# Kernel optimization log

Hardware: AMD Instinct MI355X
Metric: run time of the kernel (lower is better)

The kernel has to match this reference:

```python
import jax, jax.numpy as jnp
import numpy as np

N_NODES = 50000
N_EDGES = 800000
H, D_IN, D_OUT = 4, 256, 64


def setup_inputs() -> dict:
    key = jax.random.key(0)
    ks = jax.random.split(key, 7)
    x = jax.random.normal(ks[0], (N_NODES, D_IN), dtype=jnp.float32)
    idx = jax.random.randint(ks[1], (2, N_EDGES), 0, N_NODES, dtype=jnp.int32)
    elem = jax.random.uniform(ks[2], (N_EDGES,), dtype=jnp.float32)
    Ws = jax.random.normal(ks[3], (H, D_IN, D_OUT), dtype=jnp.float32) * 0.05
    bs = jax.random.normal(ks[4], (H, D_OUT), dtype=jnp.float32) * 0.05
    aw = jax.random.normal(ks[5], (H, 2 * D_OUT + 1), dtype=jnp.float32) * 0.05
    ab = jax.random.normal(ks[6], (H,), dtype=jnp.float32) * 0.05
    return {"x": x, "idx": idx, "elem": elem, "Ws": Ws, "bs": bs, "aw": aw, "ab": ab}


def reference(x, idx, elem, Ws, bs, aw, ab):
    N = x.shape[0]
    O = Ws.shape[-1]
    # per-head MLP (num_mlp_layers=1 -> single Linear): [H, N, O]
    feats = jnp.einsum('nd,hdo->hno', x, Ws) + bs[:, None, :]
    # attention linear on concat(src, dst, elem): split weights instead of
    # materializing the [E, 2O+1] concat; math is identical.
    aw_src, aw_dst, aw_e = aw[:, :O], aw[:, O:2 * O], aw[:, 2 * O]
    a_s = jnp.einsum('hno,ho->hn', feats, aw_src)   # [H, N]
    a_d = jnp.einsum('hno,ho->hn', feats, aw_dst)   # [H, N]
    src, dst = idx[0], idx[1]
    score = a_s[:, src] + a_d[:, dst] + aw_e[:, None] * elem[None, :] + ab[:, None]
    w = jnp.exp(-jax.nn.relu(score / 20.0))        # [H, E], in (0, 1]
    dst_f = feats[:, dst]                          # [H, E, O] gather
    seg = lambda vals: jax.ops.segment_sum(vals, src, num_segments=N)
    pooled = jax.vmap(lambda wi, fi: seg(wi[:, None] * fi))(w, dst_f)  # [H, N, O]
    row_sum = jax.vmap(lambda wi: seg(wi))(w)                          # [H, N]
    out = pooled / row_sum[:, :, None]
    # concat heads along feature dim: [N, H*O]
    return jnp.transpose(out, (1, 0, 2)).reshape(N, H * O)
```

## Files before the change

kernel.cpp:

```cpp
#include <hip/hip_runtime.h>
#include <math.h>

constexpr int DIN = 256;
constexpr int H   = 4;
constexpr int O   = 64;
constexpr int HO  = H * O;
constexpr int AWS = 2 * O + 1;
constexpr int CAP = 3072;
constexpr int HEB = 4096;

typedef __bf16 bf16x8 __attribute__((ext_vector_type(8)));
typedef __bf16 bf16x4 __attribute__((ext_vector_type(4)));
typedef float  f32x4  __attribute__((ext_vector_type(4)));

__device__ __forceinline__ float bf2f(unsigned short u) {
    union { unsigned int i; float f; } c;
    c.i = ((unsigned int)u) << 16;
    return c.f;
}

__global__ __launch_bounds__(256) void k_prep(const float* __restrict__ Ws,
    __bf16* __restrict__ Bt)
{
    const int i = blockIdx.x * 256 + threadIdx.x;
    const int k = i & 255;
    const int n = i >> 8;
    Bt[n * 256 + k] = (__bf16)Ws[(n >> 6) * (DIN * O) + k * O + (n & 63)];
}

__global__ __launch_bounds__(256) void k_gemm_hist(const float* __restrict__ x,
    const __bf16* __restrict__ Bt, const float* __restrict__ bs,
    const float* __restrict__ aw, int N, int GB,
    __bf16* __restrict__ F, float* __restrict__ a_sT, float* __restrict__ a_dT,
    const int* __restrict__ idx, int E, int* __restrict__ rank,
    int* __restrict__ hist, int NB, int NBIN)
{
    __shared__ union SM {
        __bf16 As[64][DIN + 8];
        int    lhist[64 * (DIN + 8) / 2];
    } sm;
    const int b = blockIdx.x;
    const int t = threadIdx.x;

    if (b >= GB) {
        for (int k = t; k < NBIN; k += 256) sm.lhist[k] = 0;
        __syncthreads();
        const int base_e = (b - GB) * HEB + t;
        #pragma unroll
        for (int i = 0; i < HEB / 256; ++i) {
            const int e = base_e + i * 256;
            if (e < E) {
                const int s = idx[e];
                rank[e] = atomicAdd(&sm.lhist[s >> 6], 1);
            }
        }
        __syncthreads();
        const int bh = b - GB;
        for (int k = t; k < NBIN; k += 256)
            hist[(size_t)k * NB + bh] = sm.lhist[k];
        return;
    }

    const int w    = t >> 6;
    const int lane = t & 63;
    const int c15  = lane & 15;
    const int quad = lane >> 4;
    const int n0   = b * 64;

    #pragma unroll
    for (int i = 0; i < 16; ++i) {
        const int r   = i * 4 + w;
        const int row = n0 + r;
        float4 xv = make_float4(0.f, 0.f, 0.f, 0.f);
        if (row < N) xv = *(const float4*)&x[(size_t)row * DIN + lane * 4];
        bf16x4 pv = { (__bf16)xv.x, (__bf16)xv.y, (__bf16)xv.z, (__bf16)xv.w };
        *(bf16x4*)&sm.As[r][lane * 4] = pv;
    }
    __syncthreads();

    f32x4 acc[4][4] = {};
    const __bf16* BtW = Bt + (size_t)(w * 64) * 256;
    const int kq = quad * 8;

    #pragma unroll
    for (int k0 = 0; k0 < DIN; k0 += 32) {
        bf16x8 afr[4], bfr[4];
        #pragma unroll
        for (int rt = 0; rt < 4; ++rt)
            afr[rt] = *(const bf16x8*)&sm.As[rt * 16 + c15][k0 + kq];
        #pragma unroll
        for (int ct = 0; ct < 4; ++ct)
            bfr[ct] = *(const bf16x8*)&BtW[(size_t)(ct * 16 + c15) * 256 + k0 + kq];
        #pragma unroll
        for (int rt = 0; rt < 4; ++rt)
            #pragma unroll
            for (int ct = 0; ct < 4; ++ct)
                acc[rt][ct] = __builtin_amdgcn_mfma_f32_16x16x32_bf16(
                    afr[rt], bfr[ct], acc[rt][ct], 0, 0, 0);
    }

    const int h = w;
    float bsv[4], awsv[4], awdv[4];
    #pragma unroll
    for (int ct = 0; ct < 4; ++ct) {
        const int col = ct * 16 + c15;
        bsv[ct]  = bs[w * 64 + col];
        awsv[ct] = aw[h * AWS + col];
        awdv[ct] = aw[h * AWS + O + col];
    }

    #pragma unroll
    for (int rt = 0; rt < 4; ++rt) {
        float psum[4] = {0.f, 0.f, 0.f, 0.f};
        float pdum[4] = {0.f, 0.f, 0.f, 0.f};
        #pragma unroll
        for (int ct = 0; ct < 4; ++ct) {
            #pragma unroll
            for (int reg = 0; reg < 4; ++reg) {
                const float f = acc[rt][ct][reg] + bsv[ct];
                const int row = n0 + rt * 16 + quad * 4 + reg;
                if (row < N)
                    F[(size_t)row * HO + w * 64 + ct * 16 + c15] = (__bf16)f;
                psum[reg] = fmaf(f, awsv[ct], psum[reg]);
                pdum[reg] = fmaf(f, awdv[ct], pdum[reg]);
            }
        }
        #pragma unroll
        for (int reg = 0; reg < 4; ++reg) {
            float v = psum[reg], u = pdum[reg];
            #pragma unroll
            for (int off = 1; off < 16; off <<= 1) {
                v += __shfl_xor(v, off, 64);
                u += __shfl_xor(u, off, 64);
            }
            const int row = n0 + rt * 16 + quad * 4 + reg;
            if (c15 == 0 && row < N) {
                a_sT[row * H + h] = v;
                a_dT[row * H + h] = u;
            }
        }
    }
}

__global__ __launch_bounds__(256) void k_scan1(int* __restrict__ data,
    int* __restrict__ bsum, int T)
{
    __shared__ int wsum[4], woff[4];
    const int t = threadIdx.x, b = blockIdx.x;
    const int lane = t & 63, w = t >> 6;
    const int i0 = b * 1024 + t * 4;

    int4 v = make_int4(0, 0, 0, 0);
    if (i0 + 3 < T) v = *(const int4*)&data[i0];
    else {
        if (i0     < T) v.x = data[i0];
        if (i0 + 1 < T) v.y = data[i0 + 1];
        if (i0 + 2 < T) v.z = data[i0 + 2];
    }
    const int tot = v.x + v.y + v.z + v.w;
    int s = tot;
    #pragma unroll
    for (int off = 1; off < 64; off <<= 1) {
        const int u = __shfl_up(s, off, 64);
        if (lane >= off) s += u;
    }
    if (lane == 63) wsum[w] = s;
    __syncthreads();
    if (t == 0) {
        int run = 0;
        #pragma unroll
        for (int j = 0; j < 4; ++j) { woff[j] = run; run += wsum[j]; }
        bsum[b] = run;
    }
    __syncthreads();
    const int e0 = s - tot + woff[w];
    int4 o;
    o.x = e0; o.y = e0 + v.x; o.z = o.y + v.y; o.w = o.z + v.z;
    if (i0 + 3 < T) *(int4*)&data[i0] = o;
    else {
        if (i0     < T) data[i0]     = o.x;
        if (i0 + 1 < T) data[i0 + 1] = o.y;
        if (i0 + 2 < T) data[i0 + 2] = o.z;
    }
}

__global__ __launch_bounds__(256) void k_scan2(int* __restrict__ data, int n)
{
    __shared__ int wsum[4], woff[4];
    const int t = threadIdx.x;
    const int lane = t & 63, w = t >> 6;
    const int i0 = t * 4;

    int4 v = make_int4(0, 0, 0, 0);
    if (i0 + 3 < n) v = *(const int4*)&data[i0];
    else {
        if (i0     < n) v.x = data[i0];
        if (i0 + 1 < n) v.y = data[i0 + 1];
        if (i0 + 2 < n) v.z = data[i0 + 2];
    }
    const int tot = v.x + v.y + v.z + v.w;
    int s = tot;
    #pragma unroll
    for (int off = 1; off < 64; off <<= 1) {
        const int u = __shfl_up(s, off, 64);
        if (lane >= off) s += u;
    }
    if (lane == 63) wsum[w] = s;
    __syncthreads();
    if (t == 0) {
        int run = 0;
        #pragma unroll
        for (int j = 0; j < 4; ++j) { woff[j] = run; run += wsum[j]; }
    }
    __syncthreads();
    const int e0 = s - tot + woff[w];
    int4 o;
    o.x = e0; o.y = e0 + v.x; o.z = o.y + v.y; o.w = o.z + v.z;
    if (i0 + 3 < n) *(int4*)&data[i0] = o;
    else {
        if (i0     < n) data[i0]     = o.x;
        if (i0 + 1 < n) data[i0 + 1] = o.y;
        if (i0 + 2 < n) data[i0 + 2] = o.z;
    }
}

__global__ __launch_bounds__(256) void k_scatter(const int* __restrict__ idx,
    const float* __restrict__ elem, const int* __restrict__ rank,
    const int* __restrict__ hist, const int* __restrict__ hsum,
    int NB, int E, int2* __restrict__ csr)
{
    const int e = blockIdx.x * 256 + threadIdx.x;
    if (e >= E) return;
    const int s = idx[e];
    const int d = idx[E + e];
    const int i = (s >> 6) * NB + (e / HEB);
    const int pos = hist[i] + hsum[i >> 10] + rank[e];
    csr[pos] = make_int2((int)(((unsigned)s << 16) | (unsigned)d),
                         __float_as_int(elem[e]));
}

__global__ __launch_bounds__(256) void k_binsort(const int* __restrict__ hist,
    const int* __restrict__ hsum, int NB, int NBIN, int N, int E,
    int* __restrict__ row_ptr, int2* __restrict__ csr)
{
    __shared__ int2 recs[CAP];
    __shared__ int h[64];
    __shared__ int cur[64];
    const int k = blockIdx.x;
    const int t = threadIdx.x;

    const int i0 = k * NB;
    const int S = hist[i0] + hsum[i0 >> 10];
    int Snext = E;
    if (k + 1 < NBIN) {
        const int i1 = (k + 1) * NB;
        Snext = hist[i1] + hsum[i1 >> 10];
    }
    int cnt = Snext - S;
    if (cnt > CAP) cnt = CAP;

    if (t < 64) h[t] = 0;
    __syncthreads();
    for (int j = t; j < cnt; j += 256) {
        const int2 r = csr[S + j];
        recs[j] = r;
        atomicAdd(&h[((unsigned)r.x >> 16) & 63], 1);
    }
    __syncthreads();
    if (t < 64) {
        const int v = h[t];
        int s = v;
        #pragma unroll
        for (int off = 1; off < 64; off <<= 1) {
            const int u = __shfl_up(s, off, 64);
            if (t >= off) s += u;
        }
        const int excl = s - v;
        const int node = k * 64 + t;
        if (node < N)     row_ptr[node] = S + excl;
        if (node == N - 1) row_ptr[N]   = S + excl + v;
        cur[t] = S + excl;
    }
    __syncthreads();
    for (int j = t; j < cnt; j += 256) {
        const int2 r = recs[j];
        const int pos = atomicAdd(&cur[((unsigned)r.x >> 16) & 63], 1);
        csr[pos] = make_int2((int)((unsigned)r.x & 0xFFFFu), r.y);
    }
}

__global__ __launch_bounds__(256) void k_gather(const int* __restrict__ row_ptr,
    const int2* __restrict__ csr, const float* __restrict__ a_sT,
    const float* __restrict__ a_dT, const float* __restrict__ aw,
    const float* __restrict__ ab, const __bf16* __restrict__ F,
    float* __restrict__ out, int N)
{
    __shared__ int2  s_rec[4][64];
    __shared__ float s_w[4][256];

    const int t    = threadIdx.x;
    const int wv   = t >> 6;
    const int lane = t & 63;
    const int n    = blockIdx.x * 4 + wv;
    if (n >= N) return;
    const int h16  = lane >> 4;

    const int beg = row_ptr[n];
    const int end = row_ptr[n + 1];

    const float4 as4 = *(const float4*)&a_sT[n * 4];
    const float4 ab4 = *(const float4*)&ab[0];
    const float4 awe4 = make_float4(aw[0 * AWS + 2 * O], aw[1 * AWS + 2 * O],
                                    aw[2 * AWS + 2 * O], aw[3 * AWS + 2 * O]);

    float4 acc = make_float4(0.f, 0.f, 0.f, 0.f);
    float  rs  = 0.f;
    const __bf16* __restrict__ Fl = F + lane * 4;

    for (int base = beg; base < end; base += 64) {
        const int cnt = min(64, end - base);
        if (lane < cnt) {
            const int2 r = csr[base + lane];
            s_rec[wv][lane] = r;
            const float el = __int_as_float(r.y);
            const float4 ad = *(const float4*)&a_dT[r.x * 4];
            float4 w4;
            w4.x = __expf(-fmaxf((as4.x + ad.x + awe4.x * el + ab4.x) * 0.05f, 0.f));
            w4.y = __expf(-fmaxf((as4.y + ad.y + awe4.y * el + ab4.y) * 0.05f, 0.f));
            w4.z = __expf(-fmaxf((as4.z + ad.z + awe4.z * el + ab4.z) * 0.05f, 0.f));
            w4.w = __expf(-fmaxf((as4.w + ad.w + awe4.w * el + ab4.w) * 0.05f, 0.f));
            *(float4*)&s_w[wv][lane * 4] = w4;
        }
        __threadfence_block();

        int j = 0;
        for (; j + 4 <= cnt; j += 4) {
            const int d0 = s_rec[wv][j + 0].x;
            const int d1 = s_rec[wv][j + 1].x;
            const int d2 = s_rec[wv][j + 2].x;
            const int d3 = s_rec[wv][j + 3].x;
            const float w0 = s_w[wv][(j + 0) * 4 + h16];
            const float w1 = s_w[wv][(j + 1) * 4 + h16];
            const float w2 = s_w[wv][(j + 2) * 4 + h16];
            const float w3 = s_w[wv][(j + 3) * 4 + h16];
            const ushort4 f0 = *(const ushort4*)&Fl[(size_t)d0 * HO];
            const ushort4 f1 = *(const ushort4*)&Fl[(size_t)d1 * HO];
            const ushort4 f2 = *(const ushort4*)&Fl[(size_t)d2 * HO];
            const ushort4 f3 = *(const ushort4*)&Fl[(size_t)d3 * HO];
            acc.x = fmaf(w0, bf2f(f0.x), acc.x);
            acc.y = fmaf(w0, bf2f(f0.y), acc.y);
            acc.z = fmaf(w0, bf2f(f0.z), acc.z);
            acc.w = fmaf(w0, bf2f(f0.w), acc.w);
            acc.x = fmaf(w1, bf2f(f1.x), acc.x);
            acc.y = fmaf(w1, bf2f(f1.y), acc.y);
            acc.z = fmaf(w1, bf2f(f1.z), acc.z);
            acc.w = fmaf(w1, bf2f(f1.w), acc.w);
            acc.x = fmaf(w2, bf2f(f2.x), acc.x);
            acc.y = fmaf(w2, bf2f(f2.y), acc.y);
            acc.z = fmaf(w2, bf2f(f2.z), acc.z);
            acc.w = fmaf(w2, bf2f(f2.w), acc.w);
            acc.x = fmaf(w3, bf2f(f3.x), acc.x);
            acc.y = fmaf(w3, bf2f(f3.y), acc.y);
            acc.z = fmaf(w3, bf2f(f3.z), acc.z);
            acc.w = fmaf(w3, bf2f(f3.w), acc.w);
            rs += w0 + w1 + w2 + w3;
        }
        for (; j < cnt; ++j) {
            const int d = s_rec[wv][j].x;
            const float w = s_w[wv][j * 4 + h16];
            const ushort4 fv = *(const ushort4*)&Fl[(size_t)d * HO];
            acc.x = fmaf(w, bf2f(fv.x), acc.x);
            acc.y = fmaf(w, bf2f(fv.y), acc.y);
            acc.z = fmaf(w, bf2f(fv.z), acc.z);
            acc.w = fmaf(w, bf2f(fv.w), acc.w);
            rs += w;
        }
    }

    const float inv = 1.f / rs;
    float4 o = make_float4(acc.x * inv, acc.y * inv, acc.z * inv, acc.w * inv);
    *(float4*)&out[(size_t)n * HO + lane * 4] = o;
}

extern "C" void kernel_launch(void* const* d_in, const int* in_sizes, int n_in,
                              void* d_out, int out_size, void* d_ws, size_t ws_size,
                              hipStream_t stream)
{
    const float* x    = (const float*)d_in[0];
    const int*   idx  = (const int*)d_in[1];
    const float* elem = (const float*)d_in[2];
    const float* Ws   = (const float*)d_in[3];
    const float* bs   = (const float*)d_in[4];
    const float* aw   = (const float*)d_in[5];
    const float* ab   = (const float*)d_in[6];

    const int N    = in_sizes[0] / DIN;
    const int E    = in_sizes[1] / 2;
    const int GB   = (N + 63) / 64;
    const int NB   = (E + HEB - 1) / HEB;
    const int NBIN = (N + 63) / 64;
    const int T    = NBIN * NB;
    const int nb1  = (T + 1023) / 1024;

    __bf16* F      = (__bf16*)d_ws;
    float* a_sT    = (float*)(F + (size_t)N * HO);
    float* a_dT    = a_sT + (size_t)N * H;
    int*   hist    = (int*)(a_dT + (size_t)N * H);
    int*   hsum    = hist + T;
    int*   row_ptr = hsum + (nb1 + 1);
    int*   rank    = row_ptr + (N + 1);
    size_t off = (size_t)((char*)(rank + E) - (char*)d_ws);
    off = (off + 15) & ~(size_t)15;
    int2*  csr     = (int2*)((char*)d_ws + off);
    __bf16* Bt     = (__bf16*)(csr + E);
    float* out     = (float*)d_out;

    k_prep<<<256, 256, 0, stream>>>(Ws, Bt);
    k_gemm_hist<<<GB + NB, 256, 0, stream>>>(x, Bt, bs, aw, N, GB,
                                             F, a_sT, a_dT, idx, E,
                                             rank, hist, NB, NBIN);
    k_scan1<<<nb1, 256, 0, stream>>>(hist, hsum, T);
    k_scan2<<<1, 256, 0, stream>>>(hsum, nb1);
    k_scatter<<<(E + 255) / 256, 256, 0, stream>>>(idx, elem, rank, hist,
                                                   hsum, NB, E, csr);
    k_binsort<<<NBIN, 256, 0, stream>>>(hist, hsum, NB, NBIN, N, E,
                                        row_ptr, csr);
    k_gather<<<(N + 3) / 4, 256, 0, stream>>>(row_ptr, csr, a_sT, a_dT,
                                              aw, ab, F, out, N);
}
```

Baseline: 240.3 us.

## Compute edge weights in binsort and widen gather unroll to eight edges

Edge attention weights are now computed in the binsort kernel, which already touches every edge, and written with the destination index into separate CSR arrays. The gather kernel then only loads precomputed weights instead of gathering a_dT and evaluating exp per edge. The gather inner loop is also unrolled to eight independent feature loads for more memory-level parallelism. The cost is extra global traffic: a 16-byte weight record plus a 4-byte index per edge written and read back, instead of the 8-byte record, along with more workspace and higher register pressure in gather.

```diff
diff --git a/kernel.cpp b/kernel.cpp
--- a/kernel.cpp
+++ b/kernel.cpp
@@ -241,9 +241,13 @@
 
 __global__ __launch_bounds__(256) void k_binsort(const int* __restrict__ hist,
     const int* __restrict__ hsum, int NB, int NBIN, int N, int E,
-    int* __restrict__ row_ptr, int2* __restrict__ csr)
+    const float* __restrict__ a_sT, const float* __restrict__ a_dT,
+    const float* __restrict__ aw, const float* __restrict__ ab,
+    int* __restrict__ row_ptr, const int2* __restrict__ csr,
+    int* __restrict__ csrd, float4* __restrict__ csrw)
 {
     __shared__ int2 recs[CAP];
+    __shared__ float4 s_as[64];
     __shared__ int h[64];
     __shared__ int cur[64];
     const int k = blockIdx.x;
@@ -259,7 +263,12 @@
     int cnt = Snext - S;
     if (cnt > CAP) cnt = CAP;
 
-    if (t < 64) h[t] = 0;
+    if (t < 64) {
+        h[t] = 0;
+        const int node = k * 64 + t;
+        s_as[t] = (node < N) ? *(const float4*)&a_sT[node * 4]
+                             : make_float4(0.f, 0.f, 0.f, 0.f);
+    }
     __syncthreads();
     for (int j = t; j < cnt; j += 256) {
         const int2 r = csr[S + j];
@@ -282,20 +291,35 @@
         cur[t] = S + excl;
     }
     __syncthreads();
+
+    const float4 ab4 = *(const float4*)&ab[0];
+    const float4 awe4 = make_float4(aw[0 * AWS + 2 * O], aw[1 * AWS + 2 * O],
+                                    aw[2 * AWS + 2 * O], aw[3 * AWS + 2 * O]);
+
     for (int j = t; j < cnt; j += 256) {
         const int2 r = recs[j];
-        const int pos = atomicAdd(&cur[((unsigned)r.x >> 16) & 63], 1);
-        csr[pos] = make_int2((int)((unsigned)r.x & 0xFFFFu), r.y);
+        const unsigned sd = (unsigned)r.x;
+        const int sl = (sd >> 16) & 63;
+        const int d  = (int)(sd & 0xFFFFu);
+        const int pos = atomicAdd(&cur[sl], 1);
+        const float el = __int_as_float(r.y);
+        const float4 as = s_as[sl];
+        const float4 ad = *(const float4*)&a_dT[d * 4];
+        float4 w4;
+        w4.x = __expf(-fmaxf((as.x + ad.x + awe4.x * el + ab4.x) * 0.05f, 0.f));
+        w4.y = __expf(-fmaxf((as.y + ad.y + awe4.y * el + ab4.y) * 0.05f, 0.f));
+        w4.z = __expf(-fmaxf((as.z + ad.z + awe4.z * el + ab4.z) * 0.05f, 0.f));
+        w4.w = __expf(-fmaxf((as.w + ad.w + awe4.w * el + ab4.w) * 0.05f, 0.f));
+        csrd[pos] = d;
+        csrw[pos] = w4;
     }
 }
 
 __global__ __launch_bounds__(256) void k_gather(const int* __restrict__ row_ptr,
-    const int2* __restrict__ csr, const float* __restrict__ a_sT,
-    const float* __restrict__ a_dT, const float* __restrict__ aw,
-    const float* __restrict__ ab, const __bf16* __restrict__ F,
-    float* __restrict__ out, int N)
-{
-    __shared__ int2  s_rec[4][64];
+    const int* __restrict__ csrd, const float4* __restrict__ csrw,
+    const __bf16* __restrict__ F, float* __restrict__ out, int N)
+{
+    __shared__ int   s_d[4][64];
     __shared__ float s_w[4][256];
 
     const int t    = threadIdx.x;
@@ -308,11 +332,6 @@
     const int beg = row_ptr[n];
     const int end = row_ptr[n + 1];
 
-    const float4 as4 = *(const float4*)&a_sT[n * 4];
-    const float4 ab4 = *(const float4*)&ab[0];
-    const float4 awe4 = make_float4(aw[0 * AWS + 2 * O], aw[1 * AWS + 2 * O],
-                                    aw[2 * AWS + 2 * O], aw[3 * AWS + 2 * O]);
-
     float4 acc = make_float4(0.f, 0.f, 0.f, 0.f);
     float  rs  = 0.f;
     const __bf16* __restrict__ Fl = F + lane * 4;
@@ -320,53 +339,33 @@
     for (int base = beg; base < end; base += 64) {
         const int cnt = min(64, end - base);
         if (lane < cnt) {
-            const int2 r = csr[base + lane];
-            s_rec[wv][lane] = r;
-            const float el = __int_as_float(r.y);
-            const float4 ad = *(const float4*)&a_dT[r.x * 4];
-            float4 w4;
-            w4.x = __expf(-fmaxf((as4.x + ad.x + awe4.x * el + ab4.x) * 0.05f, 0.f));
-            w4.y = __expf(-fmaxf((as4.y + ad.y + awe4.y * el + ab4.y) * 0.05f, 0.f));
-            w4.z = __expf(-fmaxf((as4.z + ad.z + awe4.z * el + ab4.z) * 0.05f, 0.f));
-            w4.w = __expf(-fmaxf((as4.w + ad.w + awe4.w * el + ab4.w) * 0.05f, 0.f));
-            *(float4*)&s_w[wv][lane * 4] = w4;
+            s_d[wv][lane] = csrd[base + lane];
+            *(float4*)&s_w[wv][lane * 4] = csrw[base + lane];
         }
         __threadfence_block();
 
         int j = 0;
-        for (; j + 4 <= cnt; j += 4) {
-            const int d0 = s_rec[wv][j + 0].x;
-            const int d1 = s_rec[wv][j + 1].x;
-            const int d2 = s_rec[wv][j + 2].x;
-            const int d3 = s_rec[wv][j + 3].x;
-            const float w0 = s_w[wv][(j + 0) * 4 + h16];
-            const float w1 = s_w[wv][(j + 1) * 4 + h16];
-            const float w2 = s_w[wv][(j + 2) * 4 + h16];
-            const float w3 = s_w[wv][(j + 3) * 4 + h16];
-            const ushort4 f0 = *(const ushort4*)&Fl[(size_t)d0 * HO];
-            const ushort4 f1 = *(const ushort4*)&Fl[(size_t)d1 * HO];
-            const ushort4 f2 = *(const ushort4*)&Fl[(size_t)d2 * HO];
-            const ushort4 f3 = *(const ushort4*)&Fl[(size_t)d3 * HO];
-            acc.x = fmaf(w0, bf2f(f0.x), acc.x);
-            acc.y = fmaf(w0, bf2f(f0.y), acc.y);
-            acc.z = fmaf(w0, bf2f(f0.z), acc.z);
-            acc.w = fmaf(w0, bf2f(f0.w), acc.w);
-            acc.x = fmaf(w1, bf2f(f1.x), acc.x);
-            acc.y = fmaf(w1, bf2f(f1.y), acc.y);
-            acc.z = fmaf(w1, bf2f(f1.z), acc.z);
-            acc.w = fmaf(w1, bf2f(f1.w), acc.w);
-            acc.x = fmaf(w2, bf2f(f2.x), acc.x);
-            acc.y = fmaf(w2, bf2f(f2.y), acc.y);
-            acc.z = fmaf(w2, bf2f(f2.z), acc.z);
-            acc.w = fmaf(w2, bf2f(f2.w), acc.w);
-            acc.x = fmaf(w3, bf2f(f3.x), acc.x);
-            acc.y = fmaf(w3, bf2f(f3.y), acc.y);
-            acc.z = fmaf(w3, bf2f(f3.z), acc.z);
-            acc.w = fmaf(w3, bf2f(f3.w), acc.w);
-            rs += w0 + w1 + w2 + w3;
+        for (; j + 8 <= cnt; j += 8) {
+            int dd[8]; float ww[8]; ushort4 ff[8];
+            #pragma unroll
+            for (int q = 0; q < 8; ++q) {
+                dd[q] = s_d[wv][j + q];
+                ww[q] = s_w[wv][(j + q) * 4 + h16];
+            }
+            #pragma unroll
+            for (int q = 0; q < 8; ++q)
+                ff[q] = *(const ushort4*)&Fl[(size_t)dd[q] * HO];
+            #pragma unroll
+            for (int q = 0; q < 8; ++q) {
+                acc.x = fmaf(ww[q], bf2f(ff[q].x), acc.x);
+                acc.y = fmaf(ww[q], bf2f(ff[q].y), acc.y);
+                acc.z = fmaf(ww[q], bf2f(ff[q].z), acc.z);
+                acc.w = fmaf(ww[q], bf2f(ff[q].w), acc.w);
+                rs += ww[q];
+            }
         }
         for (; j < cnt; ++j) {
-            const int d = s_rec[wv][j].x;
+            const int d = s_d[wv][j];
             const float w = s_w[wv][j * 4 + h16];
             const ushort4 fv = *(const ushort4*)&Fl[(size_t)d * HO];
             acc.x = fmaf(w, bf2f(fv.x), acc.x);
@@ -412,7 +411,11 @@
     size_t off = (size_t)((char*)(rank + E) - (char*)d_ws);
     off = (off + 15) & ~(size_t)15;
     int2*  csr     = (int2*)((char*)d_ws + off);
-    __bf16* Bt     = (__bf16*)(csr + E);
+    int*   csrd    = (int*)(csr + E);
+    size_t off2 = (size_t)((char*)(csrd + E) - (char*)d_ws);
+    off2 = (off2 + 15) & ~(size_t)15;
+    float4* csrw   = (float4*)((char*)d_ws + off2);
+    __bf16* Bt     = (__bf16*)(csrw + E);
     float* out     = (float*)d_out;
 
     k_prep<<<256, 256, 0, stream>>>(Ws, Bt);
@@ -424,7 +427,7 @@
     k_scatter<<<(E + 255) / 256, 256, 0, stream>>>(idx, elem, rank, hist,
                                                    hsum, NB, E, csr);
     k_binsort<<<NBIN, 256, 0, stream>>>(hist, hsum, NB, NBIN, N, E,
-                                        row_ptr, csr);
-    k_gather<<<(N + 3) / 4, 256, 0, stream>>>(row_ptr, csr, a_sT, a_dT,
-                                              aw, ab, F, out, N);
-}
+                                        a_sT, a_dT, aw, ab,
+                                        row_ptr, csr, csrd, csrw);
+    k_gather<<<(N + 3) / 4, 256, 0, stream>>>(row_ptr, csrd, csrw, F, out, N);
+}
```

Result: no change. 243.2 us (+1.2%).
